# Kernel tuning notes

Hardware: AMD Instinct MI355X
Metric: run time of the kernel (lower is better)

Reference implementation:

```python
import jax, jax.numpy as jnp
import numpy as np

LMAX = 4
S2_DIM = (LMAX + 1) ** 2                                  # 25: s2 irreps, mul 1 per l
SO3_DIM = sum((2 * l + 1) ** 2 for l in range(LMAX + 1))  # 165: so3 irreps, mul 2l+1 per l
B = 2048
F_S2, F_SO3 = 1, 16
N_S2_KERNEL = 48      # s2_healpix_grid(rec_level=1)
N_SO3_KERNEL = 192    # so3_near_identity_grid()
N_ACT_GRID = 4000     # SO3Activation resolution=10, aspect_ratio=2 -> 20x10x20, flattened
N_EVAL = 4608         # so3_healpix_grid(rec_level=2): 192 pixels x 24 gamma


def setup_inputs() -> dict:
    ks = jax.random.split(jax.random.key(0), 7)
    return {
        "x": jax.random.normal(ks[0], (B, F_S2, S2_DIM), jnp.float32),
        "w_s2": jax.random.normal(ks[1], (F_S2, F_SO3, N_S2_KERNEL), jnp.float32),
        "Y": jax.random.normal(ks[2], (N_S2_KERNEL, S2_DIM), jnp.float32),
        "w_so3": jax.random.normal(ks[3], (F_SO3, 1, N_SO3_KERNEL), jnp.float32),
        "D_kernel": jax.random.normal(ks[4], (N_SO3_KERNEL, SO3_DIM), jnp.float32),
        "D_act": jax.random.normal(ks[5], (N_ACT_GRID, SO3_DIM), jnp.float32),
        "eval_wigners": jax.random.normal(ks[6], (SO3_DIM, N_EVAL), jnp.float32) / np.sqrt(SO3_DIM),
    }


def _s2_to_so3_linear(x, psi):
    # e3nn o3.Linear(s2_irreps -> so3_irreps, f_in, f_out, external weights)
    # x:   [B, f_in, 25]  (mul 1 per degree l)
    # psi: [f_in, f_out, 25] ; column l^2+j is the weight to output-multiplicity j of degree l
    f_in, f_out = psi.shape[0], psi.shape[1]
    out, s = [], 0
    for l in range(LMAX + 1):
        d = 2 * l + 1
        x_l = x[..., s:s + d]                       # [B, f_in, d]
        p_l = psi[..., s:s + d]                     # [f_in, f_out, d] (j = out-mul idx)
        o = jnp.einsum('bxm,xyj->byjm', x_l, p_l) / np.sqrt(f_in)
        out.append(o.reshape(x.shape[0], f_out, d * d))
        s += d
    return jnp.concatenate(out, axis=-1)            # [B, f_out, 165]


def _so3_to_so3_linear(x, psi):
    # e3nn o3.Linear(so3_irreps -> so3_irreps, f_in, f_out, external weights)
    # x:   [B, f_in, 165] ; psi: [f_in, f_out, 165]
    f_in, f_out = psi.shape[0], psi.shape[1]
    out, s = [], 0
    for l in range(LMAX + 1):
        d = 2 * l + 1
        x_l = x[..., s:s + d * d].reshape(x.shape[0], f_in, d, d)   # [B,f_in,u,m]
        p_l = psi[..., s:s + d * d].reshape(f_in, f_out, d, d)      # [f_in,f_out,u,v]
        o = jnp.einsum('bxum,xyuv->byvm', x_l, p_l) / np.sqrt(f_in * d)
        out.append(o.reshape(x.shape[0], f_out, d * d))
        s += d * d
    return jnp.concatenate(out, axis=-1)            # [B, f_out, 165]


def _forward(x, w_s2, Y, w_so3, D_kernel, D_act, eval_wigners):
    # --- S2Convolution: kernel = SH-transform of grid weights, then irrep-wise linear
    psi1 = jnp.einsum('ni,xyn->xyi', Y, w_s2) / np.sqrt(N_S2_KERNEL)     # [1,16,25]
    h = _s2_to_so3_linear(x, psi1)                                        # [B,16,165]
    # --- SO3Activation: Fourier -> SO(3) grid -> relu -> Fourier
    g = jnp.einsum('bfi,gi->bfg', h, D_act) / np.sqrt(SO3_DIM)            # [B,16,4000]
    g = jax.nn.relu(g)
    h = jnp.einsum('bfg,gi->bfi', g, D_act) * (np.sqrt(SO3_DIM) / N_ACT_GRID)
    # --- SO3Convolution
    psi2 = jnp.einsum('ni,xyn->xyi', D_kernel, w_so3) / np.sqrt(N_SO3_KERNEL)  # [16,1,165]
    harmonics = _so3_to_so3_linear(h, psi2)                               # [B,1,165]
    # --- compute_probabilities: matmul with eval Wigner-D basis + softmax over grid
    probs = jax.nn.softmax(jnp.einsum('bfi,ie->be', harmonics, eval_wigners), axis=1)  # [B,4608]
    # --- top-k masking: zero out everything below the 5th-highest prob of sample 0
    fifth = jax.lax.top_k(probs, 5)[0][0, 4]
    probs = jnp.where(probs < fifth, 0.0, probs)
    return harmonics, probs


def reference(x, w_s2, Y, w_so3, D_kernel, D_act, eval_wigners):
    return _forward(x, w_s2, Y, w_so3, D_kernel, D_act, eval_wigners)
```

## Files before the change

kernel.cpp:

```cpp
#include <hip/hip_runtime.h>

typedef short bf16x8 __attribute__((ext_vector_type(8)));
typedef float f32x16 __attribute__((ext_vector_type(16)));
typedef int   i32x4  __attribute__((ext_vector_type(4)));

#define INV_SQRT165 0.07784989441615349f
#define FINAL_SCALE 0.0032113081446662823f
#define ZERO16 ((f32x16){0.f,0.f,0.f,0.f,0.f,0.f,0.f,0.f,0.f,0.f,0.f,0.f,0.f,0.f,0.f,0.f})

__device__ __forceinline__ unsigned short f2bf(float f) {
  unsigned int u = __builtin_bit_cast(unsigned int, f);
  unsigned int r = (u + 0x7FFFu + ((u >> 16) & 1u)) >> 16;
  return (unsigned short)r;
}
__device__ __forceinline__ float bf2f(unsigned short h) {
  unsigned int u = ((unsigned int)h) << 16;
  return __builtin_bit_cast(float, u);
}
__device__ __forceinline__ unsigned int pack_bf2f(float lo, float hi) {
  unsigned int a = (__builtin_bit_cast(unsigned int, lo) + 0x8000u) >> 16;
  unsigned int b = (__builtin_bit_cast(unsigned int, hi) + 0x8000u) & 0xFFFF0000u;
  return b | a;
}

__device__ __forceinline__ void gl_lds16(const void* g, void* l) {
  __builtin_amdgcn_global_load_lds(
      (const __attribute__((address_space(1))) unsigned int*)(unsigned long long)g,
      (__attribute__((address_space(3))) unsigned int*)(unsigned int)(unsigned long long)l,
      16, 0, 0);
}

__device__ __forceinline__ void decode_i(int i, int& lv, int& rel) {
  if (i < 1)       { lv = 0; rel = i; }
  else if (i < 10) { lv = 1; rel = i - 1; }
  else if (i < 35) { lv = 2; rel = i - 10; }
  else if (i < 84) { lv = 3; rel = i - 35; }
  else             { lv = 4; rel = i - 84; }
}
__device__ __forceinline__ int divq(int rel, int lv) {
  const int mag[5] = {32768, 10923, 6554, 4682, 3641};
  return (rel * mag[lv]) >> 15;
}

__device__ __forceinline__ int gperm(int p) {
  int a = p & 3, hlp = (p >> 2) & 1, c = p >> 3;
  return ((c >> 1) << 4) + hlp * 8 + ((c & 1) << 2) + a;
}

__global__ __launch_bounds__(256) void prep_k(const float* __restrict__ Da,
                                              const float* __restrict__ ew,
                                              const float* __restrict__ Y,
                                              const float* __restrict__ w_s2,
                                              const float* __restrict__ Dk,
                                              const float* __restrict__ w_so3,
                                              unsigned short* __restrict__ e1pre,
                                              unsigned short* __restrict__ d2pre,
                                              unsigned short* __restrict__ ewpre,
                                              float* __restrict__ psi2) {
  __shared__ __align__(16) unsigned short lds[13824];
  const int tid = threadIdx.x;
  const int l = tid & 63, hl = l >> 5, ln = l & 31;
  if (blockIdx.x < 512) {
    const int ci = blockIdx.x >> 2, yg = blockIdx.x & 3;
    const int g0 = ci * 32;
    float* psi1L = (float*)(lds + 6464);
    for (int e = tid; e < 6400; e += 256) lds[e] = 0;
    for (int e = tid; e < 400; e += 256) {
      int yv = e / 25, iv = e % 25;
      float s = 0.f;
      for (int n = 0; n < 48; n++) s += Y[n * 25 + iv] * w_s2[yv * 48 + n];
      psi1L[e] = s * 0.14433756729740643f;
    }
    __syncthreads();
    int rows = 4000 - g0; if (rows > 32) rows = 32; if (rows < 0) rows = 0;
    int ne = rows * 165;
    for (int e = tid; e < ne; e += 256) {
      int gl_ = e / 165, k = e - gl_ * 165;
      lds[gl_ * 200 + k] = f2bf(Da[g0 * 165 + e]);
    }
    __syncthreads();
    if (yg == 0) {
#pragma unroll
      for (int it = 0; it < 3; it++) {
        int tt = it * 4 + (tid >> 6);
        int nf = tt >> 1, gk = tt & 1;
        unsigned short v[8];
#pragma unroll
        for (int j = 0; j < 8; j++)
          v[j] = lds[(gk * 16 + hl * 8 + j) * 200 + nf * 32 + ln];
        *(i32x4*)(d2pre + ci * 6144 + tt * 512 + l * 8) = *(i32x4*)v;
      }
    }
    for (int yi = 0; yi < 4; yi++) {
      int yy = yg * 4 + yi;
#pragma unroll
      for (int it = 0; it < 4; it++) {
        int idx = it * 256 + tid;
        int kf = idx >> 9, r2 = idx & 511;
        int ll = r2 >> 3, j = r2 & 7;
        int lnn = ll & 31, hll = ll >> 5;
        int k = kf * 16 + hll * 8 + j;
        unsigned short ov = 0;
        if (k < 25) {
          int lv = (k < 1) ? 0 : (k < 4) ? 1 : (k < 9) ? 2 : (k < 16) ? 3 : 4;
          int d = 2 * lv + 1;
          int m = k - lv * lv;
          int off165 = lv * (4 * lv * lv - 1) / 3;
          int gp = gperm(lnn);
          float s = 0.f;
          const float* pr = psi1L + yy * 25 + lv * lv;
          const unsigned short* dr = lds + gp * 200 + off165 + m;
          for (int j2 = 0; j2 < d; j2++) s += pr[j2] * bf2f(dr[j2 * d]);
          ov = f2bf(s * INV_SQRT165);
        }
        e1pre[((yy * 128 + ci) * 2 + kf) * 512 + ll * 8 + j] = ov;
      }
    }
  } else if (blockIdx.x < 584) {
    const int bx2 = blockIdx.x - 512;
    const int n0 = bx2 * 64;
    for (int e = tid; e < 13824; e += 256) lds[e] = 0;
    __syncthreads();
    for (int e = tid; e < 10560; e += 256) {
      int k = e >> 6, n = e & 63;
      lds[k * 72 + n] = f2bf(ew[k * 4608 + n0 + n]);
    }
    __syncthreads();
#pragma unroll
    for (int it = 0; it < 6; it++) {
      int tb = it * 4 + (tid >> 6);
      int nt2 = tb / 12, kf = tb - nt2 * 12;
      unsigned short v[8];
#pragma unroll
      for (int j = 0; j < 8; j++)
        v[j] = lds[(kf * 16 + hl * 8 + j) * 72 + nt2 * 32 + ln];
      *(i32x4*)(ewpre + (bx2 * 2 + nt2) * 6144 + kf * 512 + l * 8) = *(i32x4*)v;
    }
  } else {
    int t = (blockIdx.x - 584) * 256 + tid;
    if (t < 2640) {
      int ch = t / 165, i = t % 165;
      float s = 0.f;
      for (int n = 0; n < 192; n++) s += Dk[n * 165 + i] * w_so3[ch * 192 + n];
      psi2[t] = s * (0.07216878364870323f * FINAL_SCALE);
    }
  }
}

__global__ __launch_bounds__(256, 3) void fused_mlp_k(
    const float* __restrict__ x,
    const unsigned short* __restrict__ e1pre,
    const unsigned short* __restrict__ d2pre,
    unsigned short* __restrict__ part)
{
  __shared__ __align__(16) unsigned char smem[24576];
  const int tid = threadIdx.x;
  const int w = tid >> 6, l = tid & 63;
  const int hl = l >> 5, ln = l & 31;
  const int h = blockIdx.x >> 8;
  const int y = (blockIdx.x >> 4) & 15;
  const int btg = blockIdx.x & 15;
  const int bt = btg * 4 + w;
  const int c0 = (h == 0) ? 0 : (h == 1) ? 43 : 86;
  const int cnt = (h == 2) ? 42 : 43;

  bf16x8 xf[2];
  {
    const float* xr = x + (bt * 32 + ln) * 25;
#pragma unroll
    for (int kf = 0; kf < 2; kf++) {
      unsigned short v[8];
#pragma unroll
      for (int j = 0; j < 8; j++) {
        int k = kf * 16 + hl * 8 + j;
        v[j] = (k < 25) ? f2bf(xr[k]) : (unsigned short)0;
      }
      xf[kf] = *(bf16x8*)v;
    }
  }

  f32x16 o[6];
#pragma unroll
  for (int i = 0; i < 6; i++) o[i] = ZERO16;

  const unsigned short* ebase = e1pre + (y * 128) * 1024;

  bf16x8 eC0 = *(const bf16x8*)(ebase + (c0 * 2 + 0) * 512 + l * 8);
  bf16x8 eC1 = *(const bf16x8*)(ebase + (c0 * 2 + 1) * 512 + l * 8);
#pragma unroll
  for (int i = 0; i < 3; i++) {
    int tb = w * 3 + i;
    gl_lds16(d2pre + c0 * 6144 + tb * 512 + l * 8, smem + tb * 1024);
  }

  for (int ci = 0; ci < cnt; ci++) {
    __syncthreads();
    const unsigned char* cb = smem + (ci & 1) * 12288;
    bf16x8 eN0 = eC0, eN1 = eC1;
    if (ci + 1 < cnt) {
      unsigned char* nb = smem + ((ci + 1) & 1) * 12288;
      const int c = c0 + ci + 1;
#pragma unroll
      for (int i = 0; i < 3; i++) {
        int tb = w * 3 + i;
        gl_lds16(d2pre + c * 6144 + tb * 512 + l * 8, nb + tb * 1024);
      }
      eN0 = *(const bf16x8*)(ebase + (c * 2 + 0) * 512 + l * 8);
      eN1 = *(const bf16x8*)(ebase + (c * 2 + 1) * 512 + l * 8);
    }
    f32x16 s = ZERO16;
    s = __builtin_amdgcn_mfma_f32_32x32x16_bf16(eC0, xf[0], s, 0, 0, 0);
    s = __builtin_amdgcn_mfma_f32_32x32x16_bf16(eC1, xf[1], s, 0, 0, 0);
    unsigned int dw[8];
#pragma unroll
    for (int p = 0; p < 8; p++)
      dw[p] = pack_bf2f(fmaxf(s[2 * p], 0.f), fmaxf(s[2 * p + 1], 0.f));
    i32x4 q0 = (i32x4){(int)dw[0], (int)dw[1], (int)dw[2], (int)dw[3]};
    i32x4 q1 = (i32x4){(int)dw[4], (int)dw[5], (int)dw[6], (int)dw[7]};
    bf16x8 a20 = __builtin_bit_cast(bf16x8, q0);
    bf16x8 a21 = __builtin_bit_cast(bf16x8, q1);
#pragma unroll
    for (int gk = 0; gk < 2; gk++) {
      bf16x8 a2 = gk ? a21 : a20;
#pragma unroll
      for (int nf = 0; nf < 6; nf++) {
        bf16x8 b2 = *(const bf16x8*)(cb + (nf * 2 + gk) * 1024 + l * 16);
        o[nf] = __builtin_amdgcn_mfma_f32_32x32x16_bf16(a2, b2, o[nf], 0, 0, 0);
      }
    }
    eC0 = eN0; eC1 = eN1;
  }

  unsigned short* pp = part + (size_t)((h * 16 + y) * 2048 + bt * 32) * 192;
#pragma unroll
  for (int nf = 0; nf < 6; nf++) {
    int n = nf * 32 + ln;
    if (n < 176) {
#pragma unroll
      for (int r = 0; r < 16; r++) {
        int row = (r & 3) + 8 * (r >> 2) + 4 * hl;
        pp[row * 192 + n] = f2bf(o[nf][r]);
      }
    }
  }
}

__global__ __launch_bounds__(256) void so3_k(const unsigned short* __restrict__ part,
                                             const float* __restrict__ psi2,
                                             float* __restrict__ harm_out,
                                             unsigned short* __restrict__ harmbpre) {
  __shared__ float lds[4 * 16 * 180];
  __shared__ float p2s[2640];
  const int tid = threadIdx.x;
  const int b0 = blockIdx.x * 4;
  for (int e = tid; e < 2640; e += 256) p2s[e] = psi2[e];
  {
    const int ybl = tid >> 2;
    const int yy = ybl & 15, bloc = ybl >> 4;
    const int s = tid & 3;
    const unsigned int* r0 = (const unsigned int*)(part + ((size_t)(0 * 16 + yy) * 2048 + b0 + bloc) * 192);
    const unsigned int* r1 = (const unsigned int*)(part + ((size_t)(1 * 16 + yy) * 2048 + b0 + bloc) * 192);
    const unsigned int* r2 = (const unsigned int*)(part + ((size_t)(2 * 16 + yy) * 2048 + b0 + bloc) * 192);
    float* dst = lds + (bloc * 16 + yy) * 180;
#pragma unroll
    for (int t = 0; t < 22; t++) {
      int d = s * 22 + t;
      if (d < 88) {
        unsigned int u0 = r0[d], u1 = r1[d], u2 = r2[d];
        int n0 = d * 2;
        dst[n0]     = bf2f((unsigned short)(u0 & 0xFFFF)) + bf2f((unsigned short)(u1 & 0xFFFF))
                    + bf2f((unsigned short)(u2 & 0xFFFF));
        dst[n0 + 1] = bf2f((unsigned short)(u0 >> 16)) + bf2f((unsigned short)(u1 >> 16))
                    + bf2f((unsigned short)(u2 >> 16));
      }
    }
  }
  __syncthreads();
  for (int jj = tid; jj < 768; jj += 256) {
    int e = (jj * 683) >> 17;
    int i = jj - e * 192;
    int bb = b0 + e;
    unsigned short* hb = harmbpre + (((bb >> 5) * 12 + (i >> 4)) << 9)
                       + ((i >> 3) & 1) * 256 + (bb & 31) * 8 + (i & 7);
    if (i < 165) {
      const float* row0 = lds + e * (16 * 180);
      int lv, rel; decode_i(i, lv, rel);
      int d = 2 * lv + 1;
      int off = i - rel;
      int v = divq(rel, lv), m = rel - v * d;
      float s = 0.f;
      for (int ch = 0; ch < 16; ch++) {
        const float* rw = row0 + ch * 180 + off;
        const float* p2 = p2s + ch * 165 + off;
        for (int u = 0; u < d; u++) s += rw[u * d + m] * p2[u * d + v];
      }
      s *= 0.25f * rsqrtf((float)d);
      harm_out[bb * 165 + i] = s;
      *hb = f2bf(s);
    } else {
      *hb = 0;
    }
  }
}

__global__ __launch_bounds__(64) void eval_k(
    const unsigned short* __restrict__ harmbpre,
    const unsigned short* __restrict__ ewpre,
    float* __restrict__ logits,
    float* __restrict__ logit0)
{
  const int l = threadIdx.x;
  const int hl = l >> 5, ln = l & 31;
  const int mt = blockIdx.y;
  const int n0 = blockIdx.x * 192;

  bf16x8 a[12];
  const short* ap = (const short*)harmbpre + mt * 6144 + l * 8;
#pragma unroll
  for (int kf = 0; kf < 12; kf++) a[kf] = *(const bf16x8*)(ap + kf * 512);

  f32x16 acc[6];
#pragma unroll
  for (int nf = 0; nf < 6; nf++) acc[nf] = ZERO16;

  const short* bp = (const short*)ewpre + (blockIdx.x * 6) * 6144 + l * 8;
#pragma unroll
  for (int kf = 0; kf < 12; kf++) {
#pragma unroll
    for (int nf = 0; nf < 6; nf++) {
      bf16x8 b = *(const bf16x8*)(bp + nf * 6144 + kf * 512);
      acc[nf] = __builtin_amdgcn_mfma_f32_32x32x16_bf16(a[kf], b, acc[nf], 0, 0, 0);
    }
  }
#pragma unroll
  for (int nf = 0; nf < 6; nf++) {
    const int col = n0 + nf * 32 + ln;
#pragma unroll
    for (int r = 0; r < 16; r++) {
      int row = (r & 3) + 8 * (r >> 2) + 4 * hl;
      logits[(mt * 32 + row) * 4608 + col] = acc[nf][r];
    }
  }
  if (mt == 0 && hl == 0) {
#pragma unroll
    for (int nf = 0; nf < 6; nf++) logit0[n0 + nf * 32 + ln] = acc[nf][0];
  }
}

__global__ __launch_bounds__(256) void fifth_k(const float* __restrict__ logit0,
                                               float* __restrict__ fifth) {
  __shared__ float buf[4608];
  __shared__ float sm[4], ss[4];
  __shared__ float wv[4]; __shared__ int wi[4];
  __shared__ float gbest;
  const int tid = threadIdx.x;
  const int l = tid & 63, w = tid >> 6;
  float v[18];
  float mx = -3.4e38f;
#pragma unroll
  for (int i = 0; i < 18; i++) {
    v[i] = logit0[i * 256 + tid];
    buf[i * 256 + tid] = v[i];
    mx = fmaxf(mx, v[i]);
  }
#pragma unroll
  for (int off = 32; off >= 1; off >>= 1) mx = fmaxf(mx, __shfl_xor(mx, off));
  if (l == 0) sm[w] = mx;
  __syncthreads();
  mx = fmaxf(fmaxf(sm[0], sm[1]), fmaxf(sm[2], sm[3]));
  float s = 0.f;
#pragma unroll
  for (int i = 0; i < 18; i++) s += __expf(v[i] - mx);
#pragma unroll
  for (int off = 32; off >= 1; off >>= 1) s += __shfl_xor(s, off);
  if (l == 0) ss[w] = s;
  __syncthreads();
  s = ss[0] + ss[1] + ss[2] + ss[3];
  float inv = 1.f / s;

  float ff = 0.f;
  for (int it = 0; it < 5; it++) {
    float bm = -3.4e38f; int bi = 0;
    for (int i = tid; i < 4608; i += 256) {
      float xx = buf[i];
      if (xx > bm) { bm = xx; bi = i; }
    }
    for (int off = 32; off >= 1; off >>= 1) {
      float ov = __shfl_xor(bm, off); int oi = __shfl_xor(bi, off);
      if (ov > bm) { bm = ov; bi = oi; }
    }
    if (l == 0) { wv[w] = bm; wi[w] = bi; }
    __syncthreads();
    if (tid == 0) {
      float B = wv[0]; int I = wi[0];
      for (int k = 1; k < 4; k++) if (wv[k] > B) { B = wv[k]; I = wi[k]; }
      gbest = B;
      buf[I] = -3.4e38f;
    }
    __syncthreads();
    ff = gbest;
    __syncthreads();
  }
  if (tid == 0) *fifth = __expf(ff - mx) * inv;
}

__global__ __launch_bounds__(256) void smthresh_k(float* __restrict__ probs,
                                                  const float* __restrict__ fifth) {
  float* p = probs + (size_t)blockIdx.x * 4608;
  const int tid = threadIdx.x;
  const int l = tid & 63, w = tid >> 6;
  __shared__ float sm[4], ss[4];
  float v[18];
  float mx = -3.4e38f;
#pragma unroll
  for (int i = 0; i < 18; i++) { v[i] = p[i * 256 + tid]; mx = fmaxf(mx, v[i]); }
#pragma unroll
  for (int off = 32; off >= 1; off >>= 1) mx = fmaxf(mx, __shfl_xor(mx, off));
  if (l == 0) sm[w] = mx;
  __syncthreads();
  mx = fmaxf(fmaxf(sm[0], sm[1]), fmaxf(sm[2], sm[3]));
  float s = 0.f;
#pragma unroll
  for (int i = 0; i < 18; i++) { v[i] = __expf(v[i] - mx); s += v[i]; }
#pragma unroll
  for (int off = 32; off >= 1; off >>= 1) s += __shfl_xor(s, off);
  if (l == 0) ss[w] = s;
  __syncthreads();
  s = ss[0] + ss[1] + ss[2] + ss[3];
  float inv = 1.f / s;
  float t = *fifth;
#pragma unroll
  for (int i = 0; i < 18; i++) {
    float pv = v[i] * inv;
    p[i * 256 + tid] = (pv < t) ? 0.f : pv;
  }
}

extern "C" void kernel_launch(void* const* d_in, const int* in_sizes, int n_in,
                              void* d_out, int out_size, void* d_ws, size_t ws_size,
                              hipStream_t stream) {
  const float* x     = (const float*)d_in[0];
  const float* w_s2  = (const float*)d_in[1];
  const float* Y     = (const float*)d_in[2];
  const float* w_so3 = (const float*)d_in[3];
  const float* Dk    = (const float*)d_in[4];
  const float* Da    = (const float*)d_in[5];
  const float* ew    = (const float*)d_in[6];

  float* out = (float*)d_out;
  float* harm_out = out;
  float* probs    = out + 337920;
  unsigned short* part = (unsigned short*)probs;

  char* ws = (char*)d_ws;
  float* psi2  = (float*)(ws + 0);
  float* fifth = (float*)(ws + 10560);
  unsigned short* e1pre    = (unsigned short*)(ws + 12288);
  unsigned short* d2pre    = (unsigned short*)(ws + 4206592);
  unsigned short* ewpre    = (unsigned short*)(ws + 5779456);
  unsigned short* harmbpre = (unsigned short*)(ws + 7548928);
  float* logit0 = (float*)(ws + 8335360);

  prep_k<<<595, 256, 0, stream>>>(Da, ew, Y, w_s2, Dk, w_so3, e1pre, d2pre, ewpre, psi2);
  fused_mlp_k<<<768, 256, 0, stream>>>(x, e1pre, d2pre, part);
  so3_k<<<512, 256, 0, stream>>>(part, psi2, harm_out, harmbpre);
  eval_k<<<dim3(24, 64), 64, 0, stream>>>(harmbpre, ewpre, probs, logit0);
  fifth_k<<<1, 256, 0, stream>>>(logit0, fifth);
  smthresh_k<<<2048, 256, 0, stream>>>(probs, fifth);
}
```

Before: 218.8 us.

## Load second-GEMM B fragments straight from global into registers, drop LDS staging

The fused MLP kernel no longer stages d2pre tiles in LDS through global_load_lds double buffering with a barrier every step. Each wave now reads its B fragments directly from global (L2-resident) into registers and uses the hardware v_cvt_pk_bf16_f32 instruction for the ReLU pack. It also raises wave priority around the MFMA burst. This removes the per-iteration __syncthreads and LDS traffic, but every wave now fetches the same d2pre data redundantly from cache. Load latency also has less overlap because there is no longer a cross-iteration prefetch of B.

```diff
diff --git a/kernel.cpp b/kernel.cpp
--- a/kernel.cpp
+++ b/kernel.cpp
@@ -16,18 +16,6 @@
 __device__ __forceinline__ float bf2f(unsigned short h) {
   unsigned int u = ((unsigned int)h) << 16;
   return __builtin_bit_cast(float, u);
-}
-__device__ __forceinline__ unsigned int pack_bf2f(float lo, float hi) {
-  unsigned int a = (__builtin_bit_cast(unsigned int, lo) + 0x8000u) >> 16;
-  unsigned int b = (__builtin_bit_cast(unsigned int, hi) + 0x8000u) & 0xFFFF0000u;
-  return b | a;
-}
-
-__device__ __forceinline__ void gl_lds16(const void* g, void* l) {
-  __builtin_amdgcn_global_load_lds(
-      (const __attribute__((address_space(1))) unsigned int*)(unsigned long long)g,
-      (__attribute__((address_space(3))) unsigned int*)(unsigned int)(unsigned long long)l,
-      16, 0, 0);
 }
 
 __device__ __forceinline__ void decode_i(int i, int& lv, int& rel) {
@@ -153,7 +141,6 @@
     const unsigned short* __restrict__ d2pre,
     unsigned short* __restrict__ part)
 {
-  __shared__ __align__(16) unsigned char smem[24576];
   const int tid = threadIdx.x;
   const int w = tid >> 6, l = tid & 63;
   const int hl = l >> 5, ln = l & 31;
@@ -183,52 +170,48 @@
 #pragma unroll
   for (int i = 0; i < 6; i++) o[i] = ZERO16;
 
-  const unsigned short* ebase = e1pre + (y * 128) * 1024;
-
-  bf16x8 eC0 = *(const bf16x8*)(ebase + (c0 * 2 + 0) * 512 + l * 8);
-  bf16x8 eC1 = *(const bf16x8*)(ebase + (c0 * 2 + 1) * 512 + l * 8);
-#pragma unroll
-  for (int i = 0; i < 3; i++) {
-    int tb = w * 3 + i;
-    gl_lds16(d2pre + c0 * 6144 + tb * 512 + l * 8, smem + tb * 1024);
-  }
+  const unsigned short* ebase = e1pre + (y * 128) * 1024 + l * 8;
+  const unsigned short* dbase = d2pre + c0 * 6144 + l * 8;
+
+  bf16x8 eC0 = *(const bf16x8*)(ebase + (c0 * 2 + 0) * 512);
+  bf16x8 eC1 = *(const bf16x8*)(ebase + (c0 * 2 + 1) * 512);
 
   for (int ci = 0; ci < cnt; ci++) {
-    __syncthreads();
-    const unsigned char* cb = smem + (ci & 1) * 12288;
-    bf16x8 eN0 = eC0, eN1 = eC1;
-    if (ci + 1 < cnt) {
-      unsigned char* nb = smem + ((ci + 1) & 1) * 12288;
-      const int c = c0 + ci + 1;
-#pragma unroll
-      for (int i = 0; i < 3; i++) {
-        int tb = w * 3 + i;
-        gl_lds16(d2pre + c * 6144 + tb * 512 + l * 8, nb + tb * 1024);
-      }
-      eN0 = *(const bf16x8*)(ebase + (c * 2 + 0) * 512 + l * 8);
-      eN1 = *(const bf16x8*)(ebase + (c * 2 + 1) * 512 + l * 8);
-    }
+    const unsigned short* db = dbase + ci * 6144;
+    bf16x8 b0[6];
+#pragma unroll
+    for (int nf = 0; nf < 6; nf++)
+      b0[nf] = *(const bf16x8*)(db + (nf * 2) * 512);
     f32x16 s = ZERO16;
     s = __builtin_amdgcn_mfma_f32_32x32x16_bf16(eC0, xf[0], s, 0, 0, 0);
     s = __builtin_amdgcn_mfma_f32_32x32x16_bf16(eC1, xf[1], s, 0, 0, 0);
+    if (ci + 1 < cnt) {
+      const int c = c0 + ci + 1;
+      eC0 = *(const bf16x8*)(ebase + (c * 2 + 0) * 512);
+      eC1 = *(const bf16x8*)(ebase + (c * 2 + 1) * 512);
+    }
     unsigned int dw[8];
 #pragma unroll
-    for (int p = 0; p < 8; p++)
-      dw[p] = pack_bf2f(fmaxf(s[2 * p], 0.f), fmaxf(s[2 * p + 1], 0.f));
+    for (int p = 0; p < 8; p++) {
+      float lo = fmaxf(s[2 * p], 0.f), hi = fmaxf(s[2 * p + 1], 0.f);
+      asm("v_cvt_pk_bf16_f32 %0, %1, %2" : "=v"(dw[p]) : "v"(lo), "v"(hi));
+    }
     i32x4 q0 = (i32x4){(int)dw[0], (int)dw[1], (int)dw[2], (int)dw[3]};
     i32x4 q1 = (i32x4){(int)dw[4], (int)dw[5], (int)dw[6], (int)dw[7]};
     bf16x8 a20 = __builtin_bit_cast(bf16x8, q0);
     bf16x8 a21 = __builtin_bit_cast(bf16x8, q1);
-#pragma unroll
-    for (int gk = 0; gk < 2; gk++) {
-      bf16x8 a2 = gk ? a21 : a20;
-#pragma unroll
-      for (int nf = 0; nf < 6; nf++) {
-        bf16x8 b2 = *(const bf16x8*)(cb + (nf * 2 + gk) * 1024 + l * 16);
-        o[nf] = __builtin_amdgcn_mfma_f32_32x32x16_bf16(a2, b2, o[nf], 0, 0, 0);
-      }
-    }
-    eC0 = eN0; eC1 = eN1;
+    bf16x8 b1[6];
+#pragma unroll
+    for (int nf = 0; nf < 6; nf++)
+      b1[nf] = *(const bf16x8*)(db + (nf * 2 + 1) * 512);
+    __builtin_amdgcn_s_setprio(1);
+#pragma unroll
+    for (int nf = 0; nf < 6; nf++)
+      o[nf] = __builtin_amdgcn_mfma_f32_32x32x16_bf16(a20, b0[nf], o[nf], 0, 0, 0);
+#pragma unroll
+    for (int nf = 0; nf < 6; nf++)
+      o[nf] = __builtin_amdgcn_mfma_f32_32x32x16_bf16(a21, b1[nf], o[nf], 0, 0, 0);
+    __builtin_amdgcn_s_setprio(0);
   }
 
   unsigned short* pp = part + (size_t)((h * 16 + y) * 2048 + bt * 32) * 192;
```

Result: slower. 251.8 us (+15.1%).
